# Optimization experiments

Hardware: AMD Instinct MI355X
Metric: run time of the kernel (lower is better)

Reference implementation:

```python
import jax, jax.numpy as jnp
import numpy as np

D_MODEL = 768
NUM_HEADS = 12
D_K = D_MODEL // NUM_HEADS
SCALE = float(np.sqrt(D_K))


def setup_inputs() -> dict:
    key = jax.random.key(0)
    ks = jax.random.split(key, 9)
    B, S, D = 2, 2048, D_MODEL
    std = 1.0 / np.sqrt(D)
    x = jax.random.normal(ks[0], (B, S, D), dtype=jnp.float32)
    attention_mask = jnp.ones((B, S), dtype=jnp.int32)
    # Linear params: weight [out, in] (torch convention), bias [out]
    Wq = jax.random.normal(ks[1], (D, D), dtype=jnp.float32) * std
    bq = jax.random.normal(ks[2], (D,), dtype=jnp.float32) * 0.01
    Wk = jax.random.normal(ks[3], (D, D), dtype=jnp.float32) * std
    bk = jax.random.normal(ks[4], (D,), dtype=jnp.float32) * 0.01
    Wv = jax.random.normal(ks[5], (D, D), dtype=jnp.float32) * std
    bv = jax.random.normal(ks[6], (D,), dtype=jnp.float32) * 0.01
    Wo = jax.random.normal(ks[7], (D, D), dtype=jnp.float32) * std
    bo = jax.random.normal(ks[8], (D,), dtype=jnp.float32) * 0.01
    return {"x": x, "attention_mask": attention_mask,
            "Wq": Wq, "bq": bq, "Wk": Wk, "bk": bk,
            "Wv": Wv, "bv": bv, "Wo": Wo, "bo": bo}


def reference(x, attention_mask, Wq, bq, Wk, bk, Wv, bv, Wo, bo):
    B, S, D = x.shape
    H, Dk = NUM_HEADS, D_K
    # QKV projections (torch Linear: x @ W.T + b)
    q = (x @ Wq.T + bq).reshape(B, S, H, Dk).transpose(0, 2, 1, 3)  # [B,H,S,Dk]
    k = (x @ Wk.T + bk).reshape(B, S, H, Dk).transpose(0, 2, 1, 3)
    v = (x @ Wv.T + bv).reshape(B, S, H, Dk).transpose(0, 2, 1, 3)
    scores = jnp.einsum('bhqd,bhkd->bhqk', q, k) / SCALE  # [B,H,S,S]
    mask = attention_mask[:, None, None, :]  # [B,1,1,S]
    scores = jnp.where(mask == 0, jnp.float32(-jnp.inf), scores)
    attn = jax.nn.softmax(scores, axis=-1)
    # dropout is identity in eval mode
    ctx = jnp.einsum('bhqk,bhkd->bhqd', attn, v)  # [B,H,S,Dk]
    ctx = ctx.transpose(0, 2, 1, 3).reshape(B, S, D)
    return ctx @ Wo.T + bo
```

## Files before the change

kernel.cpp:

```cpp
#include <hip/hip_runtime.h>
#include <stdint.h>

#define NHEAD 12
#define DKH   64
#define BB    2
#define SS    2048
#define DMOD  768
#define MTOT  (BB*SS)
#define NCHUNK 2
#define CHS   (SS/NCHUNK)
#define QBLK  128
#define NT    (CHS/64)

typedef __attribute__((ext_vector_type(8)))  _Float16 half8;
typedef __attribute__((ext_vector_type(4)))  _Float16 half4;
typedef __attribute__((ext_vector_type(2)))  __fp16   fp16x2;
typedef __attribute__((ext_vector_type(4)))  float    f32x4;
typedef __attribute__((ext_vector_type(16))) float    f32x16;

typedef __attribute__((address_space(1))) const void gv_t;
typedef __attribute__((address_space(3))) void       lv_t;

__device__ inline float fexp2(float x) { return __builtin_amdgcn_exp2f(x); }
__device__ inline int pk2(float a, float b) {
    union { fp16x2 h; int i; } u;
    u.h = __builtin_amdgcn_cvt_pkrtz(a, b);
    return u.i;
}

__global__ void k_cvt(const float* __restrict__ in, _Float16* __restrict__ out, int n) {
    int i = (blockIdx.x * 256 + threadIdx.x) * 4;
    if (i >= n) return;
    float4 v = *(const float4*)(in + i);
    half4 o;
    o.x = (_Float16)v.x; o.y = (_Float16)v.y; o.z = (_Float16)v.z; o.w = (_Float16)v.w;
    *(half4*)(out + i) = o;
}

__global__ void k_cvtw(const float* __restrict__ w0, const float* __restrict__ w1,
                       const float* __restrict__ w2, const float* __restrict__ w3,
                       _Float16* __restrict__ o0, _Float16* __restrict__ o1,
                       _Float16* __restrict__ o2, _Float16* __restrict__ o3) {
    const float* in; _Float16* out;
    switch (blockIdx.y) {
        case 0: in = w0; out = o0; break;
        case 1: in = w1; out = o1; break;
        case 2: in = w2; out = o2; break;
        default: in = w3; out = o3; break;
    }
    int i = (blockIdx.x * 256 + threadIdx.x) * 4;
    float4 v = *(const float4*)(in + i);
    half4 o;
    o.x = (_Float16)v.x; o.y = (_Float16)v.y; o.z = (_Float16)v.z; o.w = (_Float16)v.w;
    *(half4*)(out + i) = o;
}

template<int MODE>
__global__ __launch_bounds__(256, 2) void k_gemm(
    const _Float16* __restrict__ A, const _Float16* __restrict__ Bm,
    const float* __restrict__ bias0, const float* __restrict__ bias1, const float* __restrict__ bias2,
    float* __restrict__ outF,
    _Float16* __restrict__ Qd, _Float16* __restrict__ Kd, _Float16* __restrict__ Vtd,
    int K, int Ncols)
{
    __shared__ _Float16 As[128 * 32];
    __shared__ _Float16 Bs[128 * 32];
    const int tid = threadIdx.x;
    const int w = tid >> 6, l = tid & 63, lr = l & 15, lg = l >> 4;
    const int bm = blockIdx.y * 128, bn = blockIdx.x * 128;
    const int wm = (w >> 1) * 64, wn = (w & 1) * 64;
    f32x4 acc[4][4] = {};

    for (int k0 = 0; k0 < K; k0 += 32) {
        __syncthreads();
#pragma unroll
        for (int i = 0; i < 2; ++i) {
            int o = w * 2048 + i * 1024 + l * 16;
            int row = o >> 6;
            int c8  = (o >> 4) & 3;
            __builtin_amdgcn_global_load_lds(
                (gv_t*)((const char*)A + ((size_t)(bm + row) * K + k0 + c8 * 8) * 2),
                (lv_t*)((char*)As + w * 2048 + i * 1024), 16, 0, 0);
            __builtin_amdgcn_global_load_lds(
                (gv_t*)((const char*)Bm + ((size_t)(bn + row) * K + k0 + c8 * 8) * 2),
                (lv_t*)((char*)Bs + w * 2048 + i * 1024), 16, 0, 0);
        }
        __syncthreads();
        half8 af[4], bf[4];
#pragma unroll
        for (int f = 0; f < 4; ++f) {
            af[f] = *(const half8*)((const char*)As + (wm + f * 16 + lr) * 64 + lg * 16);
            bf[f] = *(const half8*)((const char*)Bs + (wn + f * 16 + lr) * 64 + lg * 16);
        }
#pragma unroll
        for (int fm = 0; fm < 4; ++fm)
#pragma unroll
            for (int fn = 0; fn < 4; ++fn)
                acc[fm][fn] = __builtin_amdgcn_mfma_f32_16x16x32_f16(af[fm], bf[fn], acc[fm][fn], 0, 0, 0);
    }

#pragma unroll
    for (int fm = 0; fm < 4; ++fm) {
#pragma unroll
        for (int fn = 0; fn < 4; ++fn) {
            int n = bn + wn + fn * 16 + lr;
            if (MODE == 0) {
                float bia = bias0[n];
#pragma unroll
                for (int j = 0; j < 4; ++j) {
                    int m = bm + wm + fm * 16 + lg * 4 + j;
                    outF[(size_t)m * Ncols + n] = acc[fm][fn][j] + bia;
                }
            } else {
                int qkv = n / 768, nn = n - qkv * 768;
                const float* bp = (qkv == 0) ? bias0 : (qkv == 1 ? bias1 : bias2);
                float bia = bp[nn];
                int h = nn >> 6, dk = nn & 63;
                int m0 = bm + wm + fm * 16 + lg * 4;
                int b = m0 >> 11;
                int s0 = m0 & 2047;
                size_t head = (size_t)b * NHEAD + h;
                if (qkv == 2) {
                    half4 pk;
#pragma unroll
                    for (int j = 0; j < 4; ++j) pk[j] = (_Float16)(acc[fm][fn][j] + bia);
                    *(half4*)(Vtd + (head * DKH + dk) * SS + s0) = pk;
                } else {
                    _Float16* dst = (qkv == 0) ? Qd : Kd;
                    float qsc = (qkv == 0) ? 0.18033688011f : 1.0f;
#pragma unroll
                    for (int j = 0; j < 4; ++j)
                        dst[(head * SS + (s0 + j)) * DKH + dk] = (_Float16)((acc[fm][fn][j] + bia) * qsc);
                }
            }
        }
    }
}

__global__ __launch_bounds__(256, 3) void k_attn(
    const _Float16* __restrict__ Qd, const _Float16* __restrict__ Kd,
    const _Float16* __restrict__ Vtd, const int* __restrict__ mask,
    _Float16* __restrict__ Opart, float* __restrict__ Mpart, float* __restrict__ Lpart)
{
    __shared__ _Float16 Ks[2 * 64 * 64];
    __shared__ _Float16 Vs[2 * 64 * 64];
    const int tid = threadIdx.x, w = tid >> 6, l = tid & 63;
    const int lq = l & 31, lhi = l >> 5;
    const int head  = blockIdx.x;
    const int qt    = blockIdx.y;
    const int chunk = blockIdx.z;
    const int b = head / NHEAD;
    const char* Qh = (const char*)(Qd + (size_t)head * SS * DKH);
    const char* Kh = (const char*)(Kd + (size_t)head * SS * DKH) + (size_t)chunk * CHS * 128;
    const char* Vh = (const char*)(Vtd + (size_t)head * DKH * SS);
    const int vcb = chunk * CHS * 2;

    const int q = qt * QBLK + w * 32 + lq;
    half8 qf[4];
#pragma unroll
    for (int kd = 0; kd < 4; ++kd)
        qf[kd] = *(const half8*)(Qh + ((size_t)q * 64 + kd * 16 + lhi * 8) * 2);

    f32x16 accO[2] = {};
    float m = -__builtin_inff(), lsum = 0.f;

    auto STAGE = [&](int kt2, int buf) {
#pragma unroll
        for (int i = 0; i < 2; ++i) {
            int o  = w * 2048 + i * 1024 + l * 16;
            int lo = o ^ (((o >> 7) & 7) << 4);
            __builtin_amdgcn_global_load_lds(
                (gv_t*)(Kh + (size_t)kt2 * 8192 + lo),
                (lv_t*)((char*)Ks + buf * 8192 + w * 2048 + i * 1024), 16, 0, 0);
            int dv = lo >> 7, inner = lo & 127;
            __builtin_amdgcn_global_load_lds(
                (gv_t*)(Vh + (size_t)dv * 4096 + vcb + kt2 * 128 + inner),
                (lv_t*)((char*)Vs + buf * 8192 + w * 2048 + i * 1024), 16, 0, 0);
        }
    };

    STAGE(0, 0);
    int cur = 0;

    for (int kt = 0; kt < NT; ++kt) {
        __syncthreads();
        if (kt < NT - 1) STAGE(kt + 1, cur ^ 1);
        int mv = mask[b * SS + chunk * CHS + kt * 64 + l];
        unsigned long long bal = __ballot(mv != 0);
        const char* kb = (const char*)Ks + cur * 8192;
        const char* vb = (const char*)Vs + cur * 8192;

        f32x16 s0 = {}, s1 = {};
#pragma unroll
        for (int kd = 0; kd < 4; ++kd) {
            int col = kd * 32 + lhi * 16;
            int ob0 = (lq * 128 + col) ^ ((lq & 7) << 4);
            half8 kf0 = *(const half8*)(kb + ob0);
            s0 = __builtin_amdgcn_mfma_f32_32x32x16_f16(kf0, qf[kd], s0, 0, 0, 0);
            int ob1 = ((32 + lq) * 128 + col) ^ ((lq & 7) << 4);
            half8 kf1 = *(const half8*)(kb + ob1);
            s1 = __builtin_amdgcn_mfma_f32_32x32x16_f16(kf1, qf[kd], s1, 0, 0, 0);
        }

        if (bal != ~0ull) {
#pragma unroll
            for (int r = 0; r < 16; ++r) {
                int kv0 = (r & 3) + 8 * (r >> 2) + 4 * lhi;
                if (!((bal >> kv0) & 1))        s0[r] = -__builtin_inff();
                if (!((bal >> (kv0 + 32)) & 1)) s1[r] = -__builtin_inff();
            }
        }

        float t[16];
#pragma unroll
        for (int i = 0; i < 16; ++i) t[i] = fmaxf(s0[i], s1[i]);
#pragma unroll
        for (int i = 0; i < 8; ++i) t[i] = fmaxf(t[i], t[i + 8]);
#pragma unroll
        for (int i = 0; i < 4; ++i) t[i] = fmaxf(t[i], t[i + 4]);
        t[0] = fmaxf(fmaxf(t[0], t[2]), fmaxf(t[1], t[3]));
        float pmax = fmaxf(t[0], __shfl_xor(t[0], 32, 64));

        if (!__all(pmax <= m + 3.0f)) {
            float mnew = fmaxf(m, pmax);
            float f = fexp2(m - mnew);
            m = mnew; lsum *= f;
            accO[0] *= f; accO[1] *= f;
        }
        float mex = fmaxf(m, -1e30f);

#pragma unroll
        for (int i = 0; i < 16; ++i) { s0[i] = fexp2(s0[i] - mex); s1[i] = fexp2(s1[i] - mex); }
#pragma unroll
        for (int i = 0; i < 16; ++i) t[i] = s0[i] + s1[i];
#pragma unroll
        for (int i = 0; i < 8; ++i) t[i] = t[i] + t[i + 8];
#pragma unroll
        for (int i = 0; i < 4; ++i) t[i] = t[i] + t[i + 4];
        t[0] = (t[0] + t[2]) + (t[1] + t[3]);
        lsum += t[0] + __shfl_xor(t[0], 32, 64);

        union PF { int w[4]; half8 h; } pf[4];
        {
            int W[8];
#pragma unroll
            for (int mm = 0; mm < 8; ++mm) W[mm] = pk2(s0[2 * mm], s0[2 * mm + 1]);
            asm("v_permlane32_swap_b32 %0, %1" : "+v"(W[0]), "+v"(W[2]));
            asm("v_permlane32_swap_b32 %0, %1" : "+v"(W[1]), "+v"(W[3]));
            asm("v_permlane32_swap_b32 %0, %1" : "+v"(W[4]), "+v"(W[6]));
            asm("v_permlane32_swap_b32 %0, %1" : "+v"(W[5]), "+v"(W[7]));
            pf[0].w[0] = W[0]; pf[0].w[1] = W[1]; pf[0].w[2] = W[2]; pf[0].w[3] = W[3];
            pf[1].w[0] = W[4]; pf[1].w[1] = W[5]; pf[1].w[2] = W[6]; pf[1].w[3] = W[7];
#pragma unroll
            for (int mm = 0; mm < 8; ++mm) W[mm] = pk2(s1[2 * mm], s1[2 * mm + 1]);
            asm("v_permlane32_swap_b32 %0, %1" : "+v"(W[0]), "+v"(W[2]));
            asm("v_permlane32_swap_b32 %0, %1" : "+v"(W[1]), "+v"(W[3]));
            asm("v_permlane32_swap_b32 %0, %1" : "+v"(W[4]), "+v"(W[6]));
            asm("v_permlane32_swap_b32 %0, %1" : "+v"(W[5]), "+v"(W[7]));
            pf[2].w[0] = W[0]; pf[2].w[1] = W[1]; pf[2].w[2] = W[2]; pf[2].w[3] = W[3];
            pf[3].w[0] = W[4]; pf[3].w[1] = W[5]; pf[3].w[2] = W[6]; pf[3].w[3] = W[7];
        }

#pragma unroll
        for (int cc = 0; cc < 4; ++cc) {
            int col = cc * 32 + lhi * 16;
#pragma unroll
            for (int ds = 0; ds < 2; ++ds) {
                int vrow = ds * 32 + lq;
                int ob = (vrow * 128 + col) ^ ((lq & 7) << 4);
                half8 vf = *(const half8*)(vb + ob);
                accO[ds] = __builtin_amdgcn_mfma_f32_32x32x16_f16(vf, pf[cc].h, accO[ds], 0, 0, 0);
            }
        }
        cur ^= 1;
    }

    const size_t prow = (size_t)(chunk * BB * NHEAD + head) * SS;
    if (lhi == 0) { Mpart[prow + q] = m; Lpart[prow + q] = lsum; }
#pragma unroll
    for (int ds = 0; ds < 2; ++ds)
#pragma unroll
        for (int rq = 0; rq < 4; ++rq) {
            half4 hv;
#pragma unroll
            for (int j = 0; j < 4; ++j) hv[j] = (_Float16)accO[ds][rq * 4 + j];
            *(half4*)(Opart + (prow + q) * DKH + ds * 32 + rq * 8 + lhi * 4) = hv;
        }
}

__global__ __launch_bounds__(256) void k_merge(
    const _Float16* __restrict__ Opart, const float* __restrict__ Mpart,
    const float* __restrict__ Lpart, _Float16* __restrict__ Ctx)
{
    int row  = blockIdx.x * 4 + (threadIdx.x >> 6);
    int lane = threadIdx.x & 63;
    int head = row >> 11, q = row & 2047;
    int b = head / NHEAD, h = head - b * NHEAD;
    float m[NCHUNK], lv[NCHUNK], M = -__builtin_inff();
#pragma unroll
    for (int c = 0; c < NCHUNK; ++c) {
        size_t pr = (size_t)(c * BB * NHEAD + head) * SS + q;
        m[c] = Mpart[pr]; lv[c] = Lpart[pr];
        M = fmaxf(M, m[c]);
    }
    float outv = 0.f;
    if (M > -1e37f) {
        float L = 0.f, acc = 0.f;
#pragma unroll
        for (int c = 0; c < NCHUNK; ++c) {
            float wgt = fexp2(m[c] - M);
            L += lv[c] * wgt;
            acc += wgt * (float)Opart[((size_t)(c * BB * NHEAD + head) * SS + q) * DKH + lane];
        }
        outv = acc / L;
    }
    Ctx[((size_t)(b * SS) + q) * DMOD + h * DKH + lane] = (_Float16)outv;
}

extern "C" void kernel_launch(void* const* d_in, const int* in_sizes, int n_in,
                              void* d_out, int out_size, void* d_ws, size_t ws_size,
                              hipStream_t stream) {
    const float* x  = (const float*)d_in[0];
    const int*  msk = (const int*)d_in[1];
    const float* Wq = (const float*)d_in[2];
    const float* bq = (const float*)d_in[3];
    const float* Wk = (const float*)d_in[4];
    const float* bk = (const float*)d_in[5];
    const float* Wv = (const float*)d_in[6];
    const float* bv = (const float*)d_in[7];
    const float* Wo = (const float*)d_in[8];
    const float* bo = (const float*)d_in[9];

    char* ws = (char*)d_ws;
    _Float16* Xb   = (_Float16*)(ws);
    _Float16* Wqkv = (_Float16*)(ws + 6291456);
    _Float16* Wob  = (_Float16*)(ws + 9830400);
    _Float16* Qd   = (_Float16*)(ws + 11010048);
    _Float16* Kd   = (_Float16*)(ws + 17301504);
    _Float16* Vtd  = (_Float16*)(ws + 23592960);
    _Float16* Ctxb = (_Float16*)(ws + 29884416);
    _Float16* Opart= (_Float16*)(ws + 36175872);
    float*    Mpart= (float*)   (ws + 48758784);
    float*    Lpart= (float*)   (ws + 49152000);

    k_cvt<<<3072, 256, 0, stream>>>(x, Xb, MTOT * DMOD);
    k_cvtw<<<dim3(576, 4), 256, 0, stream>>>(Wq, Wk, Wv, Wo,
                                             Wqkv, Wqkv + 589824, Wqkv + 1179648, Wob);

    k_gemm<1><<<dim3(18, 32), 256, 0, stream>>>(Xb, Wqkv, bq, bk, bv,
                                                nullptr, Qd, Kd, Vtd, DMOD, 0);
    k_attn<<<dim3(24, SS / QBLK, NCHUNK), 256, 0, stream>>>(Qd, Kd, Vtd, msk, Opart, Mpart, Lpart);
    k_merge<<<12288, 256, 0, stream>>>(Opart, Mpart, Lpart, Ctxb);
    k_gemm<0><<<dim3(6, 32), 256, 0, stream>>>(Ctxb, Wob, bo, nullptr, nullptr,
                                               (float*)d_out, nullptr, nullptr, nullptr,
                                               DMOD, DMOD);
}
```

Before: 115.5 us.

## Deepen GEMM K-tile with swizzled LDS, split attention into more chunks, MFMA row sums

```diff
diff --git a/kernel.cpp b/kernel.cpp
--- a/kernel.cpp
+++ b/kernel.cpp
@@ -7,7 +7,7 @@
 #define SS    2048
 #define DMOD  768
 #define MTOT  (BB*SS)
-#define NCHUNK 2
+#define NCHUNK 4
 #define CHS   (SS/NCHUNK)
 #define QBLK  128
 #define NT    (CHS/64)
@@ -63,40 +63,48 @@
     _Float16* __restrict__ Qd, _Float16* __restrict__ Kd, _Float16* __restrict__ Vtd,
     int K, int Ncols)
 {
-    __shared__ _Float16 As[128 * 32];
-    __shared__ _Float16 Bs[128 * 32];
+    __shared__ _Float16 As[128 * 64];
+    __shared__ _Float16 Bs[128 * 64];
     const int tid = threadIdx.x;
     const int w = tid >> 6, l = tid & 63, lr = l & 15, lg = l >> 4;
     const int bm = blockIdx.y * 128, bn = blockIdx.x * 128;
     const int wm = (w >> 1) * 64, wn = (w & 1) * 64;
     f32x4 acc[4][4] = {};
 
-    for (int k0 = 0; k0 < K; k0 += 32) {
+    for (int k0 = 0; k0 < K; k0 += 64) {
         __syncthreads();
 #pragma unroll
-        for (int i = 0; i < 2; ++i) {
-            int o = w * 2048 + i * 1024 + l * 16;
-            int row = o >> 6;
-            int c8  = (o >> 4) & 3;
+        for (int i = 0; i < 4; ++i) {
+            int o  = w * 4096 + i * 1024 + l * 16;
+            int lo = o ^ (((o >> 7) & 7) << 4);
+            int row = lo >> 7;
+            int colb = lo & 127;
             __builtin_amdgcn_global_load_lds(
-                (gv_t*)((const char*)A + ((size_t)(bm + row) * K + k0 + c8 * 8) * 2),
-                (lv_t*)((char*)As + w * 2048 + i * 1024), 16, 0, 0);
+                (gv_t*)((const char*)A + ((size_t)(bm + row) * K + k0) * 2 + colb),
+                (lv_t*)((char*)As + w * 4096 + i * 1024), 16, 0, 0);
             __builtin_amdgcn_global_load_lds(
-                (gv_t*)((const char*)Bm + ((size_t)(bn + row) * K + k0 + c8 * 8) * 2),
-                (lv_t*)((char*)Bs + w * 2048 + i * 1024), 16, 0, 0);
+                (gv_t*)((const char*)Bm + ((size_t)(bn + row) * K + k0) * 2 + colb),
+                (lv_t*)((char*)Bs + w * 4096 + i * 1024), 16, 0, 0);
         }
         __syncthreads();
-        half8 af[4], bf[4];
-#pragma unroll
-        for (int f = 0; f < 4; ++f) {
-            af[f] = *(const half8*)((const char*)As + (wm + f * 16 + lr) * 64 + lg * 16);
-            bf[f] = *(const half8*)((const char*)Bs + (wn + f * 16 + lr) * 64 + lg * 16);
-        }
-#pragma unroll
-        for (int fm = 0; fm < 4; ++fm)
-#pragma unroll
-            for (int fn = 0; fn < 4; ++fn)
-                acc[fm][fn] = __builtin_amdgcn_mfma_f32_16x16x32_f16(af[fm], bf[fn], acc[fm][fn], 0, 0, 0);
+#pragma unroll
+        for (int kk = 0; kk < 2; ++kk) {
+            half8 af[4], bf[4];
+#pragma unroll
+            for (int f = 0; f < 4; ++f) {
+                int ob = ((wm + f * 16 + lr) * 128 + kk * 64 + lg * 16) ^ ((lr & 7) << 4);
+                af[f] = *(const half8*)((const char*)As + ob);
+                int ob2 = ((wn + f * 16 + lr) * 128 + kk * 64 + lg * 16) ^ ((lr & 7) << 4);
+                bf[f] = *(const half8*)((const char*)Bs + ob2);
+            }
+            __builtin_amdgcn_s_setprio(1);
+#pragma unroll
+            for (int fm = 0; fm < 4; ++fm)
+#pragma unroll
+                for (int fn = 0; fn < 4; ++fn)
+                    acc[fm][fn] = __builtin_amdgcn_mfma_f32_16x16x32_f16(af[fm], bf[fn], acc[fm][fn], 0, 0, 0);
+            __builtin_amdgcn_s_setprio(0);
+        }
     }
 
 #pragma unroll
@@ -137,7 +145,7 @@
     }
 }
 
-__global__ __launch_bounds__(256, 3) void k_attn(
+__global__ __launch_bounds__(256, 4) void k_attn(
     const _Float16* __restrict__ Qd, const _Float16* __restrict__ Kd,
     const _Float16* __restrict__ Vtd, const int* __restrict__ mask,
     _Float16* __restrict__ Opart, float* __restrict__ Mpart, float* __restrict__ Lpart)
@@ -146,9 +154,12 @@
     __shared__ _Float16 Vs[2 * 64 * 64];
     const int tid = threadIdx.x, w = tid >> 6, l = tid & 63;
     const int lq = l & 31, lhi = l >> 5;
-    const int head  = blockIdx.x;
-    const int qt    = blockIdx.y;
-    const int chunk = blockIdx.z;
+    const int F = blockIdx.x;
+    const int gid = (F & 7) * 192 + (F >> 3);
+    const int head  = gid >> 6;
+    const int rem   = gid & 63;
+    const int qt    = rem >> 2;
+    const int chunk = rem & 3;
     const int b = head / NHEAD;
     const char* Qh = (const char*)(Qd + (size_t)head * SS * DKH);
     const char* Kh = (const char*)(Kd + (size_t)head * SS * DKH) + (size_t)chunk * CHS * 128;
@@ -162,7 +173,11 @@
         qf[kd] = *(const half8*)(Qh + ((size_t)q * 64 + kd * 16 + lhi * 8) * 2);
 
     f32x16 accO[2] = {};
-    float m = -__builtin_inff(), lsum = 0.f;
+    f32x16 sumA = {};
+    float m = -__builtin_inff();
+    half8 onesv;
+#pragma unroll
+    for (int i = 0; i < 8; ++i) onesv[i] = (_Float16)1.0f;
 
     auto STAGE = [&](int kt2, int buf) {
 #pragma unroll
@@ -191,6 +206,7 @@
         const char* vb = (const char*)Vs + cur * 8192;
 
         f32x16 s0 = {}, s1 = {};
+        __builtin_amdgcn_s_setprio(1);
 #pragma unroll
         for (int kd = 0; kd < 4; ++kd) {
             int col = kd * 32 + lhi * 16;
@@ -201,6 +217,7 @@
             half8 kf1 = *(const half8*)(kb + ob1);
             s1 = __builtin_amdgcn_mfma_f32_32x32x16_f16(kf1, qf[kd], s1, 0, 0, 0);
         }
+        __builtin_amdgcn_s_setprio(0);
 
         if (bal != ~0ull) {
 #pragma unroll
@@ -224,21 +241,13 @@
         if (!__all(pmax <= m + 3.0f)) {
             float mnew = fmaxf(m, pmax);
             float f = fexp2(m - mnew);
-            m = mnew; lsum *= f;
-            accO[0] *= f; accO[1] *= f;
+            m = mnew;
+            accO[0] *= f; accO[1] *= f; sumA *= f;
         }
         float mex = fmaxf(m, -1e30f);
 
 #pragma unroll
         for (int i = 0; i < 16; ++i) { s0[i] = fexp2(s0[i] - mex); s1[i] = fexp2(s1[i] - mex); }
-#pragma unroll
-        for (int i = 0; i < 16; ++i) t[i] = s0[i] + s1[i];
-#pragma unroll
-        for (int i = 0; i < 8; ++i) t[i] = t[i] + t[i + 8];
-#pragma unroll
-        for (int i = 0; i < 4; ++i) t[i] = t[i] + t[i + 4];
-        t[0] = (t[0] + t[2]) + (t[1] + t[3]);
-        lsum += t[0] + __shfl_xor(t[0], 32, 64);
 
         union PF { int w[4]; half8 h; } pf[4];
         {
@@ -261,6 +270,7 @@
             pf[3].w[0] = W[4]; pf[3].w[1] = W[5]; pf[3].w[2] = W[6]; pf[3].w[3] = W[7];
         }
 
+        __builtin_amdgcn_s_setprio(1);
 #pragma unroll
         for (int cc = 0; cc < 4; ++cc) {
             int col = cc * 32 + lhi * 16;
@@ -271,12 +281,14 @@
                 half8 vf = *(const half8*)(vb + ob);
                 accO[ds] = __builtin_amdgcn_mfma_f32_32x32x16_f16(vf, pf[cc].h, accO[ds], 0, 0, 0);
             }
-        }
+            sumA = __builtin_amdgcn_mfma_f32_32x32x16_f16(onesv, pf[cc].h, sumA, 0, 0, 0);
+        }
+        __builtin_amdgcn_s_setprio(0);
         cur ^= 1;
     }
 
     const size_t prow = (size_t)(chunk * BB * NHEAD + head) * SS;
-    if (lhi == 0) { Mpart[prow + q] = m; Lpart[prow + q] = lsum; }
+    if (lhi == 0) { Mpart[prow + q] = m; Lpart[prow + q] = sumA[0]; }
 #pragma unroll
     for (int ds = 0; ds < 2; ++ds)
 #pragma unroll
@@ -340,8 +352,8 @@
     _Float16* Vtd  = (_Float16*)(ws + 23592960);
     _Float16* Ctxb = (_Float16*)(ws + 29884416);
     _Float16* Opart= (_Float16*)(ws + 36175872);
-    float*    Mpart= (float*)   (ws + 48758784);
-    float*    Lpart= (float*)   (ws + 49152000);
+    float*    Mpart= (float*)   (ws + 61341696);
+    float*    Lpart= (float*)   (ws + 62128128);
 
     k_cvt<<<3072, 256, 0, stream>>>(x, Xb, MTOT * DMOD);
     k_cvtw<<<dim3(576, 4), 256, 0, stream>>>(Wq, Wk, Wv, Wo,
@@ -349,7 +361,7 @@
 
     k_gemm<1><<<dim3(18, 32), 256, 0, stream>>>(Xb, Wqkv, bq, bk, bv,
                                                 nullptr, Qd, Kd, Vtd, DMOD, 0);
-    k_attn<<<dim3(24, SS / QBLK, NCHUNK), 256, 0, stream>>>(Qd, Kd, Vtd, msk, Opart, Mpart, Lpart);
+    k_attn<<<dim3(24 * 16 * NCHUNK), 256, 0, stream>>>(Qd, Kd, Vtd, msk, Opart, Mpart, Lpart);
     k_merge<<<12288, 256, 0, stream>>>(Opart, Mpart, Lpart, Ctxb);
     k_gemm<0><<<dim3(6, 32), 256, 0, stream>>>(Ctxb, Wob, bo, nullptr, nullptr,
                                                (float*)d_out, nullptr, nullptr, nullptr,
```

Result: slower. 122.9 us (+6.4%).
